# Performance work log

Hardware: AMD Instinct MI355X
Metric: run time of the kernel (lower is better)

The kernel has to match this reference:

```python
import jax, jax.numpy as jnp
import numpy as np

N = 50000
E = 400000
R = 6
DIMS = (20, 256, 256, 512)


def setup_inputs() -> dict:
    key = jax.random.key(0)
    ks = jax.random.split(key, 16)
    inp = {
        "x": jax.random.normal(ks[0], (N, DIMS[0]), dtype=jnp.float32),
        "edge_index": jax.random.randint(ks[1], (2, E), 0, N, dtype=jnp.int64),
        "edge_type": jax.random.randint(ks[2], (E,), 0, R, dtype=jnp.int64),
    }
    # RGCN layer params: relation weights [R, in, out], root weight [in, out], bias [out]
    for li, (din, dout) in enumerate(zip(DIMS, DIMS[1:])):
        s = 1.0 / np.sqrt(din)
        inp[f"W{li}"] = jax.random.normal(ks[3 + 3 * li], (R, din, dout), dtype=jnp.float32) * s
        inp[f"root{li}"] = jax.random.normal(ks[4 + 3 * li], (din, dout), dtype=jnp.float32) * s
        inp[f"b{li}"] = jnp.zeros((dout,), dtype=jnp.float32)
    return inp


def _rgcn_layer(x, src, dst, etype, W, root, b):
    # Relation-specific transform of all nodes: [R, N, dout]
    h = jnp.einsum('ni,rio->rno', x, W)
    # Gather per-edge messages h[etype[e], src[e]] -> [E, dout]
    msgs = h[etype, src]
    # Mean-aggregate per (destination, relation) segment (PyG aggr='mean')
    seg = dst * R + etype  # [E]
    sums = jax.ops.segment_sum(msgs, seg, num_segments=N * R)          # [N*R, dout]
    cnt = jax.ops.segment_sum(jnp.ones((msgs.shape[0],), x.dtype), seg, num_segments=N * R)
    mean = sums / jnp.maximum(cnt, 1.0)[:, None]
    agg = mean.reshape(N, R, -1).sum(axis=1)  # sum over relations
    return agg + x @ root + b


def reference(x, edge_index, edge_type, W0, root0, b0, W1, root1, b1, W2, root2, b2):
    src, dst = edge_index[0], edge_index[1]  # messages flow source -> target
    params = ((W0, root0, b0), (W1, root1, b1), (W2, root2, b2))
    h = x
    for (W, root, b) in params:
        h = _rgcn_layer(h, src, dst, edge_type, W, root, b)
        h = jax.nn.relu(h)
    h = jnp.tanh(h)
    z = jnp.max(h, axis=0)          # graph-level max pool over nodes -> [latent]
    z = z / jnp.linalg.norm(z)      # normalized latent space
    return z[None, :]               # [1, latent]
```

## Files before the change

kernel.cpp:

```cpp
#include <hip/hip_runtime.h>

#define N_NODES 50000
#define N_EDGES 400000
#define N_REL 6
#define NSEG (N_NODES * N_REL)
#define NTILE ((N_NODES + 63) / 64)

#define SCAN_TILE 1024
#define SCAN_NB ((NSEG + SCAN_TILE - 1) / SCAN_TILE)

typedef float4 f4;
typedef short bf16x8 __attribute__((ext_vector_type(8)));
typedef float f32x4 __attribute__((ext_vector_type(4)));
typedef float f32x16 __attribute__((ext_vector_type(16)));
typedef int i32x8 __attribute__((ext_vector_type(8)));

typedef __attribute__((address_space(1))) const void gvoid_t;
typedef __attribute__((address_space(3))) void lvoid_t;

__device__ __forceinline__ void gl_lds16(const void* g, void* l) {
    __builtin_amdgcn_global_load_lds((gvoid_t*)g, (lvoid_t*)l, 16, 0, 0);
}

__device__ __forceinline__ unsigned enc_f32(float f) {
    unsigned u = __float_as_uint(f);
    return (u & 0x80000000u) ? ~u : (u | 0x80000000u);
}
__device__ __forceinline__ float dec_f32(unsigned e) {
    return __uint_as_float((e & 0x80000000u) ? (e ^ 0x80000000u) : ~e);
}
__device__ __forceinline__ unsigned short bf16_rne(float x) {
    unsigned u = __float_as_uint(x);
    return (unsigned short)((u + 0x7FFFu + ((u >> 16) & 1u)) >> 16);
}
__device__ __forceinline__ unsigned fp8x4(float a0, float a1, float a2, float a3) {
    unsigned r = __builtin_amdgcn_cvt_pk_fp8_f32(a0, a1, 0, 0);
    r = __builtin_amdgcn_cvt_pk_fp8_f32(a2, a3, r, 1);
    return r;
}
__device__ __forceinline__ unsigned char fp8_1(float v) {
    return (unsigned char)(__builtin_amdgcn_cvt_pk_fp8_f32(v, v, 0, 0) & 0xFF);
}

#define SWZ(row, slot) ((size_t)(row) * 32 + (((slot) ^ (((row) >> 1) & 3)) * 8))

__global__ void count_seg(const int* __restrict__ ei, const int* __restrict__ et,
                          int* __restrict__ cnt) {
    int e = blockIdx.x * blockDim.x + threadIdx.x;
    if (e < N_EDGES) atomicAdd(&cnt[ei[N_EDGES + e] * N_REL + et[e]], 1);
}

__global__ void scan1(int* __restrict__ cnt, int* __restrict__ bsum) {
    __shared__ int sh[256];
    int t = threadIdx.x, b = blockIdx.x;
    int base = b * SCAN_TILE + t * 4;
    int v[4]; int s = 0;
    #pragma unroll
    for (int i = 0; i < 4; ++i) {
        v[i] = (base + i < NSEG) ? cnt[base + i] : 0;
        s += v[i];
    }
    sh[t] = s; __syncthreads();
    for (int o = 1; o < 256; o <<= 1) {
        int x = (t >= o) ? sh[t - o] : 0;
        __syncthreads();
        sh[t] += x;
        __syncthreads();
    }
    int run = sh[t] - s;
    #pragma unroll
    for (int i = 0; i < 4; ++i) {
        if (base + i < NSEG) cnt[base + i] = run;
        run += v[i];
    }
    if (t == 255) bsum[b] = sh[255];
}

__global__ void scan2(int* __restrict__ bsum) {
    __shared__ int sh[512];
    int t = threadIdx.x;
    int v = (t < SCAN_NB) ? bsum[t] : 0;
    sh[t] = v; __syncthreads();
    for (int o = 1; o < 512; o <<= 1) {
        int x = (t >= o) ? sh[t - o] : 0;
        __syncthreads();
        sh[t] += x;
        __syncthreads();
    }
    if (t < SCAN_NB) bsum[t] = sh[t] - v;
}

__global__ void scan3(const int* __restrict__ part, const int* __restrict__ bsum,
                      int* __restrict__ rowptr, int* __restrict__ fillptr) {
    int t = threadIdx.x, b = blockIdx.x;
    int base = b * SCAN_TILE + t * 4;
    int off = bsum[b];
    #pragma unroll
    for (int i = 0; i < 4; ++i) {
        if (base + i < NSEG) {
            int v = part[base + i] + off;
            rowptr[base + i] = v;
            fillptr[base + i] = v;
        }
    }
    if (b == 0 && t == 0) rowptr[NSEG] = N_EDGES;
}

__global__ void fill_edges(const int* __restrict__ ei, const int* __restrict__ et,
                           int* __restrict__ fillptr, int* __restrict__ esrc) {
    int e = blockIdx.x * blockDim.x + threadIdx.x;
    if (e < N_EDGES) {
        int seg = ei[N_EDGES + e] * N_REL + et[e];
        int p = atomicAdd(&fillptr[seg], 1);
        esrc[p] = ei[e];
    }
}

__global__ void rcp_kernel(const int* __restrict__ rowptr, float* __restrict__ rcp) {
    int s = blockIdx.x * blockDim.x + threadIdx.x;
    if (s < NSEG) {
        int c = rowptr[s + 1] - rowptr[s];
        rcp[s] = 1.0f / (float)(c > 1 ? c : 1);
    }
}

__global__ void prep_w0(const float* __restrict__ Wf, const float* __restrict__ rootW,
                        unsigned short* __restrict__ Wt,
                        int K1, int din, int dout, int KB) {
    int k = blockIdx.x;
    int n = blockIdx.y * 256 + threadIdx.x;
    if (n >= dout) return;
    float v = 0.f;
    if (k < K1) v = Wf[(size_t)k * dout + n];
    else if (k < K1 + din) v = rootW[(size_t)(k - K1) * dout + n];
    Wt[(size_t)n * KB + k] = bf16_rne(v);
}

__global__ void prep_wpk8(const float* __restrict__ Wf, const float* __restrict__ rootW,
                          unsigned char* __restrict__ Wpk, int K1, int dout) {
    int k = blockIdx.x;
    int ct = blockIdx.y;
    int nl = threadIdx.x;
    int col = ct * 256 + nl;
    float v = (k < K1) ? Wf[(size_t)k * dout + col]
                       : rootW[(size_t)(k - K1) * dout + col];
    v *= 16.0f;
    int p = k >> 6;
    Wpk[((size_t)(ct * 28 + p)) * 16384 + (size_t)nl * 64 + (k & 63)] = fp8_1(v);
}

__global__ void gather0(const float* __restrict__ x, const int* __restrict__ rowptr,
                        const int* __restrict__ esrc, const float* __restrict__ rcp,
                        unsigned short* __restrict__ Abf0) {
    int idx = blockIdx.x * blockDim.x + threadIdx.x;
    if (idx >= NSEG * 5) return;
    int s = idx / 5, q = idx - s * 5;
    float ax = 0.f, ay = 0.f, az = 0.f, aw = 0.f;
    int e0 = rowptr[s], e1 = rowptr[s + 1];
    for (int e = e0; e < e1; ++e) {
        const f4 u = *(const f4*)&x[(size_t)esrc[e] * 20 + q * 4];
        ax += u.x; ay += u.y; az += u.z; aw += u.w;
    }
    float sc = rcp[s];
    int node = s / N_REL, rel = s - node * N_REL;
    unsigned short* p = &Abf0[(size_t)node * 160 + rel * 20 + q * 4];
    unsigned o0 = bf16_rne(ax * sc) | ((unsigned)bf16_rne(ay * sc) << 16);
    unsigned o1 = bf16_rne(az * sc) | ((unsigned)bf16_rne(aw * sc) << 16);
    *(unsigned*)(p + 0) = o0;
    *(unsigned*)(p + 2) = o1;
}

__global__ void copyx0(const float* __restrict__ x, unsigned short* __restrict__ Abf0) {
    int t = blockIdx.x * blockDim.x + threadIdx.x;
    int n = t >> 5, d = t & 31;
    if (n >= N_NODES || d >= 20) return;
    Abf0[(size_t)n * 160 + 120 + d] = bf16_rne(x[(size_t)n * 20 + d]);
}

__global__ void gather_all8(const unsigned char* __restrict__ h8, const int* __restrict__ rowptr,
                            const int* __restrict__ esrc, const float* __restrict__ rcp,
                            unsigned char* __restrict__ Apk) {
    int t = blockIdx.x * blockDim.x + threadIdx.x;
    int sl = t >> 3;
    int q = t & 7;
    if (sl < NSEG) {
        int e0 = rowptr[sl], e1 = rowptr[sl + 1];
        float a[32];
        #pragma unroll
        for (int i = 0; i < 32; ++i) a[i] = 0.f;
        for (int e = e0; e < e1; ++e) {
            const unsigned char* hp = &h8[(size_t)esrc[e] * 256 + q * 32];
            #pragma unroll
            for (int c = 0; c < 2; ++c) {
                int4 v = *(const int4*)&hp[c * 16];
                const unsigned* pu = (const unsigned*)&v;
                #pragma unroll
                for (int j = 0; j < 4; ++j) {
                    unsigned u = pu[j];
                    a[c * 16 + j * 4 + 0] += __builtin_amdgcn_cvt_f32_fp8(u, 0);
                    a[c * 16 + j * 4 + 1] += __builtin_amdgcn_cvt_f32_fp8(u, 1);
                    a[c * 16 + j * 4 + 2] += __builtin_amdgcn_cvt_f32_fp8(u, 2);
                    a[c * 16 + j * 4 + 3] += __builtin_amdgcn_cvt_f32_fp8(u, 3);
                }
            }
        }
        float sc = rcp[sl];
        int node = sl / 6, rel = sl - node * 6;
        int rt = node >> 6, m = node & 63;
        int ks = rel * 8 + q;
        unsigned ow[8];
        #pragma unroll
        for (int i = 0; i < 8; ++i)
            ow[i] = fp8x4(a[4 * i] * sc, a[4 * i + 1] * sc, a[4 * i + 2] * sc, a[4 * i + 3] * sc);
        int p = ks >> 1, sp = ks & 1;
        unsigned char* dst = Apk + ((size_t)(rt * 28 + p)) * 4096 + (size_t)m * 64;
        int rot = (m >> 1) & 3;
        *(int4*)(dst + (((sp * 2 + 0 + rot) & 3) * 16)) = make_int4(ow[0], ow[1], ow[2], ow[3]);
        *(int4*)(dst + (((sp * 2 + 1 + rot) & 3) * 16)) = make_int4(ow[4], ow[5], ow[6], ow[7]);
    } else if (sl < NSEG + N_NODES) {
        int node = sl - NSEG;
        int rt = node >> 6, m = node & 63;
        const unsigned char* hp = &h8[(size_t)node * 256 + q * 32];
        int4 lo = *(const int4*)(hp + 0);
        int4 hi = *(const int4*)(hp + 16);
        int ks = 48 + q;
        int p = ks >> 1, sp = ks & 1;
        unsigned char* dst = Apk + ((size_t)(rt * 28 + p)) * 4096 + (size_t)m * 64;
        int rot = (m >> 1) & 3;
        *(int4*)(dst + (((sp * 2 + 0 + rot) & 3) * 16)) = lo;
        *(int4*)(dst + (((sp * 2 + 1 + rot) & 3) * 16)) = hi;
    }
}

__global__ __launch_bounds__(256)
void gemm_l0(const unsigned short* __restrict__ A, const unsigned short* __restrict__ Wt,
             const float* __restrict__ bias, unsigned char* __restrict__ outH8,
             int Ktot, int KB, int dout) {
    __shared__ unsigned short As[64 * 32];
    __shared__ unsigned short Bs[256 * 32];
    const int tid = threadIdx.x;
    const int col0 = blockIdx.x * 256;
    const int row0 = blockIdx.y * 64;
    const int w = tid >> 6, l = tid & 63;
    f32x4 acc[4][4] = {};

    for (int k0 = 0; k0 < Ktot; k0 += 32) {
        {
            int m = tid >> 2, slot = tid & 3;
            int4 v = {0, 0, 0, 0};
            int mg = row0 + m;
            if (mg < N_NODES) v = *(const int4*)&A[(size_t)mg * Ktot + k0 + slot * 8];
            *(int4*)&As[SWZ(m, slot)] = v;
        }
        {
            int nb = tid >> 2, slot = tid & 3;
            #pragma unroll
            for (int j = 0; j < 4; ++j) {
                int n = nb + j * 64;
                int4 v = *(const int4*)&Wt[(size_t)(col0 + n) * KB + k0 + slot * 8];
                *(int4*)&Bs[SWZ(n, slot)] = v;
            }
        }
        __syncthreads();
        bf16x8 af[4], bfr[4];
        #pragma unroll
        for (int rf = 0; rf < 4; ++rf)
            af[rf] = *(const bf16x8*)&As[SWZ(rf * 16 + (l & 15), l >> 4)];
        #pragma unroll
        for (int cf = 0; cf < 4; ++cf)
            bfr[cf] = *(const bf16x8*)&Bs[SWZ(w * 64 + cf * 16 + (l & 15), l >> 4)];
        #pragma unroll
        for (int cf = 0; cf < 4; ++cf)
            #pragma unroll
            for (int rf = 0; rf < 4; ++rf)
                acc[rf][cf] = __builtin_amdgcn_mfma_f32_16x16x32_bf16(
                    af[rf], bfr[cf], acc[rf][cf], 0, 0, 0);
        __syncthreads();
    }

    const int colbase = col0 + w * 64;
    #pragma unroll
    for (int cf = 0; cf < 4; ++cf) {
        int c = colbase + cf * 16 + (l & 15);
        float bb = bias[c];
        #pragma unroll
        for (int rf = 0; rf < 4; ++rf)
            #pragma unroll
            for (int i = 0; i < 4; ++i) {
                int m = row0 + rf * 16 + (l >> 4) * 4 + i;
                if (m < N_NODES) {
                    float v = fmaxf(acc[rf][cf][i] + bb, 0.f);
                    outH8[(size_t)m * dout + c] = fp8_1(v);
                }
            }
    }
}

__global__ __launch_bounds__(256, 3)
void gemm_mx(const unsigned char* __restrict__ Apk, const unsigned char* __restrict__ Wpk,
             const float* __restrict__ bias, unsigned char* __restrict__ outH8,
             unsigned* __restrict__ maxbuf, int dout, int fuse) {
    __shared__ __align__(16) unsigned char As[2][16384];
    __shared__ unsigned lmax[256];

    const int tid = threadIdx.x;
    const int w = tid >> 6, l = tid & 63;
    const int row0 = blockIdx.y * 64;
    const int bcol = blockIdx.x * 256;
    const int cg0 = bcol + w * 64;
    const int ctIdx = cg0 >> 8;
    const int nOff = cg0 & 255;

    f32x16 acc[2][2] = {};

    const unsigned char* aBlock = Apk + (size_t)blockIdx.y * 28 * 4096;
    const unsigned char* bLane = Wpk + (size_t)ctIdx * 28 * 16384
                               + (size_t)(nOff + (l & 31)) * 64 + (size_t)(l >> 5) * 32;

    auto stage = [&](int S, int buf) {
        #pragma unroll
        for (int i = 0; i < 4; ++i) {
            int c = w * 4 + i;
            gl_lds16(aBlock + (size_t)S * 16384 + (size_t)c * 1024 + l * 16,
                     &As[buf][c * 1024]);
        }
    };
    auto readA = [&](int buf, int q, i32x8 (&A2)[2]) {
        #pragma unroll
        for (int rf = 0; rf < 2; ++rf) {
            int mrow = rf * 32 + (l & 31);
            int rot = (mrow >> 1) & 3;
            int g = (l >> 5) * 2;
            const unsigned char* base = &As[buf][q * 4096 + (size_t)mrow * 64];
            int4 lo = *(const int4*)(base + (((g + 0 + rot) & 3) * 16));
            int4 hi = *(const int4*)(base + (((g + 1 + rot) & 3) * 16));
            i32x8 r;
            r[0] = lo.x; r[1] = lo.y; r[2] = lo.z; r[3] = lo.w;
            r[4] = hi.x; r[5] = hi.y; r[6] = hi.z; r[7] = hi.w;
            A2[rf] = r;
        }
    };
    auto loadB = [&](int p, i32x8 (&B2)[2]) {
        #pragma unroll
        for (int cf = 0; cf < 2; ++cf) {
            const unsigned char* bp = bLane + (size_t)p * 16384 + (size_t)cf * 2048;
            int4 lo = *(const int4*)bp;
            int4 hi = *(const int4*)(bp + 16);
            i32x8 r;
            r[0] = lo.x; r[1] = lo.y; r[2] = lo.z; r[3] = lo.w;
            r[4] = hi.x; r[5] = hi.y; r[6] = hi.z; r[7] = hi.w;
            B2[cf] = r;
        }
    };
    auto domfma = [&](i32x8 (&A2)[2], i32x8 (&B2)[2]) {
        #pragma unroll
        for (int cf = 0; cf < 2; ++cf)
            #pragma unroll
            for (int rf = 0; rf < 2; ++rf)
                acc[rf][cf] = __builtin_amdgcn_mfma_scale_f32_32x32x64_f8f6f4(
                    A2[rf], B2[cf], acc[rf][cf], 0, 0, 0, 127, 0, 123);
    };

    i32x8 aX[2], aY[2], bX[2], bY[2];

    stage(0, 0);
    loadB(0, bX);

    for (int S = 0; S < 7; ++S) {
        const int buf = S & 1;
        const int P0 = S * 4;
        __syncthreads();
        readA(buf, 0, aX);
        readA(buf, 1, aY); loadB(P0 + 1, bY); domfma(aX, bX);
        readA(buf, 2, aX); loadB(P0 + 2, bX); domfma(aY, bY);
        readA(buf, 3, aY); loadB(P0 + 3, bY); domfma(aX, bX);
        if (P0 + 4 < 28) loadB(P0 + 4, bX);
        if (S < 6) stage(S + 1, buf ^ 1);
        domfma(aY, bY);
    }

    if (!fuse) {
        #pragma unroll
        for (int cf = 0; cf < 2; ++cf) {
            int c = cg0 + cf * 32 + (l & 31);
            float bb = bias[c];
            #pragma unroll
            for (int rf = 0; rf < 2; ++rf)
                #pragma unroll
                for (int reg = 0; reg < 16; ++reg) {
                    int m = row0 + rf * 32 + (reg & 3) + 8 * (reg >> 2) + 4 * (l >> 5);
                    if (m < N_NODES) {
                        float v = fmaxf(acc[rf][cf][reg] + bb, 0.f);
                        outH8[(size_t)m * dout + c] = fp8_1(v);
                    }
                }
        }
    } else {
        lmax[tid] = 0u;
        __syncthreads();
        #pragma unroll
        for (int cf = 0; cf < 2; ++cf) {
            int c = cg0 + cf * 32 + (l & 31);
            float bb = bias[c];
            float mv = 0.f;
            bool any = false;
            #pragma unroll
            for (int rf = 0; rf < 2; ++rf)
                #pragma unroll
                for (int reg = 0; reg < 16; ++reg) {
                    int m = row0 + rf * 32 + (reg & 3) + 8 * (reg >> 2) + 4 * (l >> 5);
                    if (m < N_NODES) {
                        float v = acc[rf][cf][reg] + bb;
                        mv = any ? fmaxf(mv, v) : v;
                        any = true;
                    }
                }
            if (any) atomicMax(&lmax[c - bcol], enc_f32(mv));
        }
        __syncthreads();
        atomicMax(&maxbuf[bcol + tid], lmax[tid]);
    }
}

__global__ void finalize_kernel(const unsigned* __restrict__ maxbuf,
                                float* __restrict__ out) {
    __shared__ float red[8];
    int c = threadIdx.x;
    float v = dec_f32(maxbuf[c]);
    v = fmaxf(v, 0.0f);
    float t = tanhf(v);
    float s = t * t;
    #pragma unroll
    for (int o = 32; o > 0; o >>= 1) s += __shfl_down(s, o);
    int wid = c >> 6;
    if ((c & 63) == 0) red[wid] = s;
    __syncthreads();
    if (c < 8) {
        float wsum = red[c];
        #pragma unroll
        for (int o = 4; o > 0; o >>= 1) wsum += __shfl_down(wsum, o);
        if (c == 0) red[0] = wsum;
    }
    __syncthreads();
    float norm = sqrtf(red[0]);
    out[c] = t / norm;
}

static inline size_t align_up(size_t v, size_t a) { return (v + a - 1) / a * a; }

extern "C" void kernel_launch(void* const* d_in, const int* in_sizes, int n_in,
                              void* d_out, int out_size, void* d_ws, size_t ws_size,
                              hipStream_t stream) {
    const float* x  = (const float*)d_in[0];
    const int*   ei = (const int*)d_in[1];
    const int*   et = (const int*)d_in[2];
    const float* W0 = (const float*)d_in[3];
    const float* r0 = (const float*)d_in[4];
    const float* b0 = (const float*)d_in[5];
    const float* W1 = (const float*)d_in[6];
    const float* r1 = (const float*)d_in[7];
    const float* b1 = (const float*)d_in[8];
    const float* W2 = (const float*)d_in[9];
    const float* r2 = (const float*)d_in[10];
    const float* b2 = (const float*)d_in[11];
    float* out = (float*)d_out;

    char* ws = (char*)d_ws;
    size_t off = 0;
    int* cntpart = (int*)(ws + off); off = align_up(off + (size_t)NSEG * 4, 256);
    int* bsum = (int*)(ws + off);    off = align_up(off + 512 * 4, 256);
    int* rowptr = (int*)(ws + off);  off = align_up(off + (size_t)(NSEG + 1) * 4, 256);
    int* fillptr = (int*)(ws + off); off = align_up(off + (size_t)NSEG * 4, 256);
    int* esrc = (int*)(ws + off);    off = align_up(off + (size_t)N_EDGES * 4, 256);
    float* rcp = (float*)(ws + off); off = align_up(off + (size_t)NSEG * 4, 256);
    unsigned* maxbuf = (unsigned*)(ws + off); off = align_up(off + 512 * 4, 256);
    unsigned short* Wt0 = (unsigned short*)(ws + off); off = align_up(off + (size_t)256 * 160 * 2, 256);
    unsigned char* Wpk1 = (unsigned char*)(ws + off); off = align_up(off + (size_t)1 * 28 * 16384, 256);
    unsigned char* Wpk2 = (unsigned char*)(ws + off); off = align_up(off + (size_t)2 * 28 * 16384, 256);
    unsigned char* hbuf1 = (unsigned char*)(ws + off); off = align_up(off + (size_t)N_NODES * 256, 256);
    unsigned char* hbuf2 = (unsigned char*)(ws + off); off = align_up(off + (size_t)N_NODES * 256, 256);
    unsigned short* Abf0 = (unsigned short*)(ws + off); off = align_up(off + (size_t)N_NODES * 160 * 2, 256);
    unsigned char* Apk = (unsigned char*)(ws + off); off = align_up(off + (size_t)NTILE * 28 * 4096, 256);
    if (ws_size < off) return;

    hipMemsetAsync(cntpart, 0, (size_t)NSEG * 4, stream);
    count_seg<<<(N_EDGES + 255) / 256, 256, 0, stream>>>(ei, et, cntpart);
    scan1<<<SCAN_NB, 256, 0, stream>>>(cntpart, bsum);
    scan2<<<1, 512, 0, stream>>>(bsum);
    scan3<<<SCAN_NB, 256, 0, stream>>>(cntpart, bsum, rowptr, fillptr);
    rcp_kernel<<<(NSEG + 255) / 256, 256, 0, stream>>>(rowptr, rcp);
    fill_edges<<<(N_EDGES + 255) / 256, 256, 0, stream>>>(ei, et, fillptr, esrc);
    hipMemsetAsync(maxbuf, 0, 512 * 4, stream);

    prep_w0<<<dim3(160, 1), 256, 0, stream>>>(W0, r0, Wt0, 120, 20, 256, 160);
    prep_wpk8<<<dim3(1792, 1), 256, 0, stream>>>(W1, r1, Wpk1, 1536, 256);
    prep_wpk8<<<dim3(1792, 2), 256, 0, stream>>>(W2, r2, Wpk2, 1536, 512);

    hipMemsetAsync(Abf0, 0, (size_t)N_NODES * 160 * 2, stream);
    gather0<<<(NSEG * 5 + 255) / 256, 256, 0, stream>>>(x, rowptr, esrc, rcp, Abf0);
    copyx0<<<(N_NODES * 32 + 255) / 256, 256, 0, stream>>>(x, Abf0);
    gemm_l0<<<dim3(1, NTILE), 256, 0, stream>>>(Abf0, Wt0, b0, hbuf1, 160, 160, 256);

    const int gthreads = (NSEG + N_NODES) * 8;

    gather_all8<<<(gthreads + 255) / 256, 256, 0, stream>>>(hbuf1, rowptr, esrc, rcp, Apk);
    gemm_mx<<<dim3(1, NTILE), 256, 0, stream>>>(Apk, Wpk1, b1, hbuf2, nullptr, 256, 0);

    gather_all8<<<(gthreads + 255) / 256, 256, 0, stream>>>(hbuf2, rowptr, esrc, rcp, Apk);
    gemm_mx<<<dim3(2, NTILE), 256, 0, stream>>>(Apk, Wpk2, b2, nullptr, maxbuf, 512, 1);

    finalize_kernel<<<1, 512, 0, stream>>>(maxbuf, out);
}
```

Measured before the change: 299.9 us.

## Triple-buffer A tiles and hand-schedule B loads with explicit vmcnt waits in gemm_mx

Moves the MX-fp8 GEMM's A-operand LDS staging from double to triple buffering so global-to-LDS copies run two stages ahead. B-operand loads become inline-asm global_load_dwordx4 with explicit vmcnt waits and sched_barriers, plus s_setprio around the MFMA groups. The loop is fully unrolled through macros. The aim is to hide global memory latency behind MFMA work, at the cost of more LDS per block (which may lower occupancy) and fragile hand-counted waitcnt values.

```diff
diff --git a/kernel.cpp b/kernel.cpp
--- a/kernel.cpp
+++ b/kernel.cpp
@@ -14,6 +14,7 @@
 typedef float f32x4 __attribute__((ext_vector_type(4)));
 typedef float f32x16 __attribute__((ext_vector_type(16)));
 typedef int i32x8 __attribute__((ext_vector_type(8)));
+typedef int i32x4 __attribute__((ext_vector_type(4)));
 
 typedef __attribute__((address_space(1))) const void gvoid_t;
 typedef __attribute__((address_space(3))) void lvoid_t;
@@ -300,7 +301,7 @@
 void gemm_mx(const unsigned char* __restrict__ Apk, const unsigned char* __restrict__ Wpk,
              const float* __restrict__ bias, unsigned char* __restrict__ outH8,
              unsigned* __restrict__ maxbuf, int dout, int fuse) {
-    __shared__ __align__(16) unsigned char As[2][16384];
+    __shared__ __align__(16) unsigned char As[3][16384];
     __shared__ unsigned lmax[256];
 
     const int tid = threadIdx.x;
@@ -312,72 +313,120 @@
     const int nOff = cg0 & 255;
 
     f32x16 acc[2][2] = {};
+    i32x8 aF[2];
+    i32x4 bq[2][4];
 
     const unsigned char* aBlock = Apk + (size_t)blockIdx.y * 28 * 4096;
     const unsigned char* bLane = Wpk + (size_t)ctIdx * 28 * 16384
                                + (size_t)(nOff + (l & 31)) * 64 + (size_t)(l >> 5) * 32;
 
-    auto stage = [&](int S, int buf) {
-        #pragma unroll
-        for (int i = 0; i < 4; ++i) {
-            int c = w * 4 + i;
-            gl_lds16(aBlock + (size_t)S * 16384 + (size_t)c * 1024 + l * 16,
-                     &As[buf][c * 1024]);
-        }
-    };
-    auto readA = [&](int buf, int q, i32x8 (&A2)[2]) {
-        #pragma unroll
-        for (int rf = 0; rf < 2; ++rf) {
-            int mrow = rf * 32 + (l & 31);
-            int rot = (mrow >> 1) & 3;
-            int g = (l >> 5) * 2;
-            const unsigned char* base = &As[buf][q * 4096 + (size_t)mrow * 64];
-            int4 lo = *(const int4*)(base + (((g + 0 + rot) & 3) * 16));
-            int4 hi = *(const int4*)(base + (((g + 1 + rot) & 3) * 16));
-            i32x8 r;
-            r[0] = lo.x; r[1] = lo.y; r[2] = lo.z; r[3] = lo.w;
-            r[4] = hi.x; r[5] = hi.y; r[6] = hi.z; r[7] = hi.w;
-            A2[rf] = r;
-        }
-    };
-    auto loadB = [&](int p, i32x8 (&B2)[2]) {
-        #pragma unroll
-        for (int cf = 0; cf < 2; ++cf) {
-            const unsigned char* bp = bLane + (size_t)p * 16384 + (size_t)cf * 2048;
-            int4 lo = *(const int4*)bp;
-            int4 hi = *(const int4*)(bp + 16);
-            i32x8 r;
-            r[0] = lo.x; r[1] = lo.y; r[2] = lo.z; r[3] = lo.w;
-            r[4] = hi.x; r[5] = hi.y; r[6] = hi.z; r[7] = hi.w;
-            B2[cf] = r;
-        }
-    };
-    auto domfma = [&](i32x8 (&A2)[2], i32x8 (&B2)[2]) {
-        #pragma unroll
-        for (int cf = 0; cf < 2; ++cf)
-            #pragma unroll
-            for (int rf = 0; rf < 2; ++rf)
-                acc[rf][cf] = __builtin_amdgcn_mfma_scale_f32_32x32x64_f8f6f4(
-                    A2[rf], B2[cf], acc[rf][cf], 0, 0, 0, 127, 0, 123);
-    };
-
-    i32x8 aX[2], aY[2], bX[2], bY[2];
-
-    stage(0, 0);
-    loadB(0, bX);
-
-    for (int S = 0; S < 7; ++S) {
-        const int buf = S & 1;
-        const int P0 = S * 4;
-        __syncthreads();
-        readA(buf, 0, aX);
-        readA(buf, 1, aY); loadB(P0 + 1, bY); domfma(aX, bX);
-        readA(buf, 2, aX); loadB(P0 + 2, bX); domfma(aY, bY);
-        readA(buf, 3, aY); loadB(P0 + 3, bY); domfma(aX, bX);
-        if (P0 + 4 < 28) loadB(P0 + 4, bX);
-        if (S < 6) stage(S + 1, buf ^ 1);
-        domfma(aY, bY);
-    }
+#define SB() __builtin_amdgcn_sched_barrier(0)
+
+#define STAGE(g, buf) do {                                                   \
+        _Pragma("unroll")                                                    \
+        for (int i = 0; i < 4; ++i) {                                        \
+            int c = w * 4 + i;                                               \
+            gl_lds16(aBlock + (size_t)(g) * 16384 + (size_t)c * 1024 + l * 16, \
+                     &As[buf][c * 1024]);                                    \
+        }                                                                    \
+    } while (0)
+
+#define LOADB(p, s) do {                                                     \
+        const unsigned char* _bp = bLane + (size_t)(p) * 16384;              \
+        asm volatile("global_load_dwordx4 %0, %1, off"                       \
+                     : "=&v"(bq[s][0]) : "v"(_bp));                          \
+        asm volatile("global_load_dwordx4 %0, %1, off offset:16"             \
+                     : "=&v"(bq[s][1]) : "v"(_bp));                          \
+        asm volatile("global_load_dwordx4 %0, %1, off offset:2048"           \
+                     : "=&v"(bq[s][2]) : "v"(_bp));                          \
+        asm volatile("global_load_dwordx4 %0, %1, off offset:2064"           \
+                     : "=&v"(bq[s][3]) : "v"(_bp));                          \
+    } while (0)
+
+#define READA(buf, q) do {                                                   \
+        _Pragma("unroll")                                                    \
+        for (int rf = 0; rf < 2; ++rf) {                                     \
+            int mrow = rf * 32 + (l & 31);                                   \
+            int rot = (mrow >> 1) & 3;                                       \
+            int g = (l >> 5) * 2;                                            \
+            const unsigned char* base = &As[buf][(q) * 4096 + (size_t)mrow * 64]; \
+            i32x4 lo = *(const i32x4*)(base + (((g + 0 + rot) & 3) * 16));   \
+            i32x4 hi = *(const i32x4*)(base + (((g + 1 + rot) & 3) * 16));   \
+            i32x8 r;                                                         \
+            r[0] = lo[0]; r[1] = lo[1]; r[2] = lo[2]; r[3] = lo[3];          \
+            r[4] = hi[0]; r[5] = hi[1]; r[6] = hi[2]; r[7] = hi[3];          \
+            aF[rf] = r;                                                      \
+        }                                                                    \
+    } while (0)
+
+#define DOMFMA(s) do {                                                       \
+        i32x8 Bq0, Bq1;                                                      \
+        Bq0[0] = bq[s][0][0]; Bq0[1] = bq[s][0][1];                          \
+        Bq0[2] = bq[s][0][2]; Bq0[3] = bq[s][0][3];                          \
+        Bq0[4] = bq[s][1][0]; Bq0[5] = bq[s][1][1];                          \
+        Bq0[6] = bq[s][1][2]; Bq0[7] = bq[s][1][3];                          \
+        Bq1[0] = bq[s][2][0]; Bq1[1] = bq[s][2][1];                          \
+        Bq1[2] = bq[s][2][2]; Bq1[3] = bq[s][2][3];                          \
+        Bq1[4] = bq[s][3][0]; Bq1[5] = bq[s][3][1];                          \
+        Bq1[6] = bq[s][3][2]; Bq1[7] = bq[s][3][3];                          \
+        acc[0][0] = __builtin_amdgcn_mfma_scale_f32_32x32x64_f8f6f4(         \
+            aF[0], Bq0, acc[0][0], 0, 0, 0, 127, 0, 123);                    \
+        acc[1][0] = __builtin_amdgcn_mfma_scale_f32_32x32x64_f8f6f4(         \
+            aF[1], Bq0, acc[1][0], 0, 0, 0, 127, 0, 123);                    \
+        acc[0][1] = __builtin_amdgcn_mfma_scale_f32_32x32x64_f8f6f4(         \
+            aF[0], Bq1, acc[0][1], 0, 0, 0, 127, 0, 123);                    \
+        acc[1][1] = __builtin_amdgcn_mfma_scale_f32_32x32x64_f8f6f4(         \
+            aF[1], Bq1, acc[1][1], 0, 0, 0, 127, 0, 123);                    \
+    } while (0)
+
+#define PHASE(buf, q, s, WN, p) do {                                         \
+        READA(buf, q);                                                       \
+        asm volatile("s_waitcnt vmcnt(" WN ")");                             \
+        SB();                                                                \
+        __builtin_amdgcn_s_setprio(1);                                       \
+        DOMFMA(s);                                                           \
+        __builtin_amdgcn_s_setprio(0);                                       \
+        SB();                                                                \
+        LOADB(p, s);                                                         \
+        SB();                                                                \
+    } while (0)
+
+#define SSTEP(S, TW) do {                                                    \
+        asm volatile("s_waitcnt vmcnt(" TW ")");                             \
+        SB();                                                                \
+        __builtin_amdgcn_s_barrier();                                        \
+        SB();                                                                \
+        PHASE((S) % 3, 0, 0, "8", 4 * (S) + 2 <= 27 ? 4 * (S) + 2 : 27);     \
+        PHASE((S) % 3, 1, 1, "8", 4 * (S) + 3 <= 27 ? 4 * (S) + 3 : 27);     \
+        PHASE((S) % 3, 2, 0, "4", 4 * (S) + 4 <= 27 ? 4 * (S) + 4 : 27);     \
+        PHASE((S) % 3, 3, 1, "4", 4 * (S) + 5 <= 27 ? 4 * (S) + 5 : 27);     \
+        STAGE((S) + 2 <= 6 ? (S) + 2 : 6, ((S) + 2) % 3);                    \
+        SB();                                                                \
+    } while (0)
+
+    STAGE(0, 0);
+    SB();
+    LOADB(0, 0);
+    LOADB(1, 1);
+    SB();
+    STAGE(1, 1);
+    SB();
+
+    SSTEP(0, "12");
+    SSTEP(1, "20");
+    SSTEP(2, "20");
+    SSTEP(3, "20");
+    SSTEP(4, "20");
+    SSTEP(5, "20");
+    SSTEP(6, "20");
+
+#undef SSTEP
+#undef PHASE
+#undef DOMFMA
+#undef READA
+#undef LOADB
+#undef STAGE
+#undef SB
 
     if (!fuse) {
         #pragma unroll
```

Measured after the change: 308.3 us. +2.8%, slower.

## Replace LDS-staged A tiles with direct register prefetch pipeline in fp8 GEMM

Applied to the files above, without the earlier changes.

Removes the LDS double-buffer and global_load_lds staging for the A operand in gemm_mx. Each lane now loads its A and B fragments straight from global memory into a 3-deep register ring, fully unrolled over the 28 K-steps. The launch becomes a 1D grid with a swizzled block order for the fused layer, so blocks sharing an A row tile run close together and hit L2. This drops the per-stage barriers and LDS traffic, but raises register pressure (launch bounds relaxed) and makes every wave re-read A from global/L2.

```diff
diff --git a/kernel.cpp b/kernel.cpp
--- a/kernel.cpp
+++ b/kernel.cpp
@@ -14,13 +14,7 @@
 typedef float f32x4 __attribute__((ext_vector_type(4)));
 typedef float f32x16 __attribute__((ext_vector_type(16)));
 typedef int i32x8 __attribute__((ext_vector_type(8)));
-
-typedef __attribute__((address_space(1))) const void gvoid_t;
-typedef __attribute__((address_space(3))) void lvoid_t;
-
-__device__ __forceinline__ void gl_lds16(const void* g, void* l) {
-    __builtin_amdgcn_global_load_lds((gvoid_t*)g, (lvoid_t*)l, 16, 0, 0);
-}
+typedef int i32x4 __attribute__((ext_vector_type(4)));
 
 __device__ __forceinline__ unsigned enc_f32(float f) {
     unsigned u = __float_as_uint(f);
@@ -296,88 +290,90 @@
     }
 }
 
-__global__ __launch_bounds__(256, 3)
+__global__ __launch_bounds__(256)
 void gemm_mx(const unsigned char* __restrict__ Apk, const unsigned char* __restrict__ Wpk,
              const float* __restrict__ bias, unsigned char* __restrict__ outH8,
              unsigned* __restrict__ maxbuf, int dout, int fuse) {
-    __shared__ __align__(16) unsigned char As[2][16384];
     __shared__ unsigned lmax[256];
 
     const int tid = threadIdx.x;
     const int w = tid >> 6, l = tid & 63;
-    const int row0 = blockIdx.y * 64;
-    const int bcol = blockIdx.x * 256;
+    int by, bx;
+    if (fuse) {
+        int hw = blockIdx.x;
+        if (hw < 1552) { by = ((hw >> 4) << 3) | (hw & 7); bx = (hw >> 3) & 1; }
+        else { int r = hw - 1552; by = 776 + (r % 6); bx = r / 6; }
+    } else {
+        by = blockIdx.x; bx = 0;
+    }
+    const int row0 = by * 64;
+    const int bcol = bx * 256;
     const int cg0 = bcol + w * 64;
     const int ctIdx = cg0 >> 8;
     const int nOff = cg0 & 255;
 
-    f32x16 acc[2][2] = {};
-
-    const unsigned char* aBlock = Apk + (size_t)blockIdx.y * 28 * 4096;
+    const unsigned char* aT = Apk + (size_t)by * 28 * 4096;
     const unsigned char* bLane = Wpk + (size_t)ctIdx * 28 * 16384
                                + (size_t)(nOff + (l & 31)) * 64 + (size_t)(l >> 5) * 32;
-
-    auto stage = [&](int S, int buf) {
-        #pragma unroll
-        for (int i = 0; i < 4; ++i) {
-            int c = w * 4 + i;
-            gl_lds16(aBlock + (size_t)S * 16384 + (size_t)c * 1024 + l * 16,
-                     &As[buf][c * 1024]);
-        }
-    };
-    auto readA = [&](int buf, int q, i32x8 (&A2)[2]) {
-        #pragma unroll
-        for (int rf = 0; rf < 2; ++rf) {
-            int mrow = rf * 32 + (l & 31);
-            int rot = (mrow >> 1) & 3;
-            int g = (l >> 5) * 2;
-            const unsigned char* base = &As[buf][q * 4096 + (size_t)mrow * 64];
-            int4 lo = *(const int4*)(base + (((g + 0 + rot) & 3) * 16));
-            int4 hi = *(const int4*)(base + (((g + 1 + rot) & 3) * 16));
-            i32x8 r;
-            r[0] = lo.x; r[1] = lo.y; r[2] = lo.z; r[3] = lo.w;
-            r[4] = hi.x; r[5] = hi.y; r[6] = hi.z; r[7] = hi.w;
-            A2[rf] = r;
-        }
-    };
-    auto loadB = [&](int p, i32x8 (&B2)[2]) {
-        #pragma unroll
-        for (int cf = 0; cf < 2; ++cf) {
-            const unsigned char* bp = bLane + (size_t)p * 16384 + (size_t)cf * 2048;
-            int4 lo = *(const int4*)bp;
-            int4 hi = *(const int4*)(bp + 16);
-            i32x8 r;
-            r[0] = lo.x; r[1] = lo.y; r[2] = lo.z; r[3] = lo.w;
-            r[4] = hi.x; r[5] = hi.y; r[6] = hi.z; r[7] = hi.w;
-            B2[cf] = r;
-        }
-    };
-    auto domfma = [&](i32x8 (&A2)[2], i32x8 (&B2)[2]) {
-        #pragma unroll
-        for (int cf = 0; cf < 2; ++cf)
-            #pragma unroll
-            for (int rf = 0; rf < 2; ++rf)
-                acc[rf][cf] = __builtin_amdgcn_mfma_scale_f32_32x32x64_f8f6f4(
-                    A2[rf], B2[cf], acc[rf][cf], 0, 0, 0, 127, 0, 123);
-    };
-
-    i32x8 aX[2], aY[2], bX[2], bY[2];
-
-    stage(0, 0);
-    loadB(0, bX);
-
-    for (int S = 0; S < 7; ++S) {
-        const int buf = S & 1;
-        const int P0 = S * 4;
-        __syncthreads();
-        readA(buf, 0, aX);
-        readA(buf, 1, aY); loadB(P0 + 1, bY); domfma(aX, bX);
-        readA(buf, 2, aX); loadB(P0 + 2, bX); domfma(aY, bY);
-        readA(buf, 3, aY); loadB(P0 + 3, bY); domfma(aX, bX);
-        if (P0 + 4 < 28) loadB(P0 + 4, bX);
-        if (S < 6) stage(S + 1, buf ^ 1);
-        domfma(aY, bY);
-    }
+    const int rot = (l >> 1) & 3;
+    const int g = (l >> 5) * 2;
+    const int o00 = (l & 31) * 64 + (((g + 0 + rot) & 3) * 16);
+    const int o01 = (l & 31) * 64 + (((g + 1 + rot) & 3) * 16);
+    const int o10 = o00 + 2048;
+    const int o11 = o01 + 2048;
+
+    f32x16 acc[2][2] = {};
+    i32x4 A0[3], A1[3], A2[3], A3[3];
+    i32x4 B0[3], B1[3], B2[3], B3[3];
+
+#define LOADP(p, s) do {                                                     \
+        const unsigned char* _ap = aT + (size_t)(p) * 4096;                  \
+        const unsigned char* _bp = bLane + (size_t)(p) * 16384;              \
+        A0[s] = *(const i32x4*)(_ap + o00);                                  \
+        A1[s] = *(const i32x4*)(_ap + o01);                                  \
+        A2[s] = *(const i32x4*)(_ap + o10);                                  \
+        A3[s] = *(const i32x4*)(_ap + o11);                                  \
+        B0[s] = *(const i32x4*)(_bp + 0);                                    \
+        B1[s] = *(const i32x4*)(_bp + 16);                                   \
+        B2[s] = *(const i32x4*)(_bp + 2048);                                 \
+        B3[s] = *(const i32x4*)(_bp + 2064);                                 \
+    } while (0)
+
+#define DOP(s) do {                                                          \
+        i32x8 a0 = __builtin_shufflevector(A0[s], A1[s], 0,1,2,3,4,5,6,7);   \
+        i32x8 a1 = __builtin_shufflevector(A2[s], A3[s], 0,1,2,3,4,5,6,7);   \
+        i32x8 b0 = __builtin_shufflevector(B0[s], B1[s], 0,1,2,3,4,5,6,7);   \
+        i32x8 b1 = __builtin_shufflevector(B2[s], B3[s], 0,1,2,3,4,5,6,7);   \
+        acc[0][0] = __builtin_amdgcn_mfma_scale_f32_32x32x64_f8f6f4(         \
+            a0, b0, acc[0][0], 0, 0, 0, 127, 0, 123);                        \
+        acc[1][0] = __builtin_amdgcn_mfma_scale_f32_32x32x64_f8f6f4(         \
+            a1, b0, acc[1][0], 0, 0, 0, 127, 0, 123);                        \
+        acc[0][1] = __builtin_amdgcn_mfma_scale_f32_32x32x64_f8f6f4(         \
+            a0, b1, acc[0][1], 0, 0, 0, 127, 0, 123);                        \
+        acc[1][1] = __builtin_amdgcn_mfma_scale_f32_32x32x64_f8f6f4(         \
+            a1, b1, acc[1][1], 0, 0, 0, 127, 0, 123);                        \
+    } while (0)
+
+#define STEP(p) do {                                                         \
+        DOP((p) % 3);                                                        \
+        if ((p) + 3 < 28) LOADP((p) + 3, (p) % 3);                           \
+    } while (0)
+
+    LOADP(0, 0);
+    LOADP(1, 1);
+    LOADP(2, 2);
+
+    STEP(0);  STEP(1);  STEP(2);  STEP(3);
+    STEP(4);  STEP(5);  STEP(6);  STEP(7);
+    STEP(8);  STEP(9);  STEP(10); STEP(11);
+    STEP(12); STEP(13); STEP(14); STEP(15);
+    STEP(16); STEP(17); STEP(18); STEP(19);
+    STEP(20); STEP(21); STEP(22); STEP(23);
+    STEP(24); STEP(25); STEP(26); STEP(27);
+
+#undef STEP
+#undef DOP
+#undef LOADP
 
     if (!fuse) {
         #pragma unroll
@@ -504,10 +500,10 @@
     const int gthreads = (NSEG + N_NODES) * 8;
 
     gather_all8<<<(gthreads + 255) / 256, 256, 0, stream>>>(hbuf1, rowptr, esrc, rcp, Apk);
-    gemm_mx<<<dim3(1, NTILE), 256, 0, stream>>>(Apk, Wpk1, b1, hbuf2, nullptr, 256, 0);
+    gemm_mx<<<dim3(NTILE), 256, 0, stream>>>(Apk, Wpk1, b1, hbuf2, nullptr, 256, 0);
 
     gather_all8<<<(gthreads + 255) / 256, 256, 0, stream>>>(hbuf2, rowptr, esrc, rcp, Apk);
-    gemm_mx<<<dim3(2, NTILE), 256, 0, stream>>>(Apk, Wpk2, b2, nullptr, maxbuf, 512, 1);
+    gemm_mx<<<dim3(2 * NTILE), 256, 0, stream>>>(Apk, Wpk2, b2, nullptr, maxbuf, 512, 1);
 
     finalize_kernel<<<1, 512, 0, stream>>>(maxbuf, out);
 }
```

Measured after the change: 344.2 us. 14.8% more time.
